# Performance work log

Measured on AMD Instinct MI355X. Metric: run time of the kernel, lower is better.

The kernel has to match this reference:

```python
import jax, jax.numpy as jnp
import numpy as np

B, S, D = 2, 2048, 2048
H, KVH, HD = 32, 8, 64
GROUPS = H // KVH  # 4
NEG = -1e9


def setup_inputs() -> dict:
    key = jax.random.key(0)
    ks = jax.random.split(key, 5)
    x = jax.random.normal(ks[0], (B, S, D), dtype=jnp.float32)
    # causal additive mask [1,1,S,S]
    causal = jnp.triu(jnp.full((S, S), NEG, dtype=jnp.float32), k=1)[None, None]
    Wq = jax.random.normal(ks[1], (D, D), dtype=jnp.float32) * (D ** -0.5)
    Wk = jax.random.normal(ks[2], (KVH * HD, D), dtype=jnp.float32) * (D ** -0.5)
    Wv = jax.random.normal(ks[3], (KVH * HD, D), dtype=jnp.float32) * (D ** -0.5)
    Wo = jax.random.normal(ks[4], (D, D), dtype=jnp.float32) * (D ** -0.5)
    return {"x": x, "attention_mask": causal, "Wq": Wq, "Wk": Wk, "Wv": Wv, "Wo": Wo}


def reference(x, attention_mask, Wq, Wk, Wv, Wo):
    b, s, _ = x.shape
    # projections (nn.Linear: y = x @ W.T)
    q = (x @ Wq.T).reshape(b, s, H, HD).transpose(0, 2, 1, 3)      # [b,H,s,hd]
    k = (x @ Wk.T).reshape(b, s, KVH, HD).transpose(0, 2, 1, 3)    # [b,KVH,s,hd]
    v = (x @ Wv.T).reshape(b, s, KVH, HD).transpose(0, 2, 1, 3)
    new_kv_cache = (k, v)
    # repeat_interleave over head dim for GQA
    k = jnp.repeat(k, GROUPS, axis=1)  # [b,H,s,hd]
    v = jnp.repeat(v, GROUPS, axis=1)
    scale = 1.0 / jnp.sqrt(jnp.float32(HD))
    scores = jnp.einsum('bhqd,bhkd->bhqk', q, k) * scale
    scores = scores + attention_mask
    attn = jax.nn.softmax(scores.astype(jnp.float32), axis=-1).astype(q.dtype)
    out = jnp.einsum('bhqk,bhkd->bhqd', attn, v)  # [b,H,s,hd]
    out = out.transpose(0, 2, 1, 3).reshape(b, s, H * HD)
    output = out @ Wo.T
    return (output, new_kv_cache[0], new_kv_cache[1])
```

## Files before the change

kernel.cpp:

```cpp
#include <hip/hip_runtime.h>
#include <hip/hip_bf16.h>
#include <stdint.h>

#define B_ 2
#define S_ 2048
#define D_ 2048
#define H_ 32
#define KVH_ 8
#define HD_ 64

typedef __bf16 bf16x8 __attribute__((ext_vector_type(8)));
typedef float f32x4 __attribute__((ext_vector_type(4)));

#define MFMA16(a, b, c) __builtin_amdgcn_mfma_f32_16x16x32_bf16((a), (b), (c), 0, 0, 0)

typedef __attribute__((address_space(1))) void gvoid_t;
typedef __attribute__((address_space(3))) void lvoid_t;

__device__ __forceinline__ void async_ld16(__hip_bfloat16* lds, const __hip_bfloat16* g) {
  __builtin_amdgcn_global_load_lds((gvoid_t*)(void*)(g), (lvoid_t*)(lds), 16, 0, 0);
}

__device__ __forceinline__ unsigned short f2bu(float f) {
  __hip_bfloat16 h = __float2bfloat16(f);
  return *reinterpret_cast<unsigned short*>(&h);
}

__global__ void cast_all_kernel(const float* __restrict__ x,
                                const float* __restrict__ wq,
                                const float* __restrict__ wk,
                                const float* __restrict__ wv,
                                const float* __restrict__ wo,
                                unsigned short* __restrict__ xb,
                                unsigned short* __restrict__ wqkvb,
                                unsigned short* __restrict__ wob) {
  constexpr int NX = B_ * S_ * D_ / 4;
  constexpr int NQ = D_ * D_ / 4;
  constexpr int NK = KVH_ * HD_ * D_ / 4;
  constexpr int E0 = NX;
  constexpr int E1 = E0 + NQ;
  constexpr int E2 = E1 + NK;
  constexpr int E3 = E2 + NK;
  constexpr int E4 = E3 + NQ;
  const int stride = gridDim.x * blockDim.x;
  for (int i = blockIdx.x * blockDim.x + threadIdx.x; i < E4; i += stride) {
    const float* src; unsigned short* dst; int j;
    if (i < E0)      { src = x;  dst = xb;                              j = i; }
    else if (i < E1) { src = wq; dst = wqkvb;                           j = i - E0; }
    else if (i < E2) { src = wk; dst = wqkvb + (size_t)2048 * D_;       j = i - E1; }
    else if (i < E3) { src = wv; dst = wqkvb + (size_t)2560 * D_;       j = i - E2; }
    else             { src = wo; dst = wob;                             j = i - E3; }
    float4 v = reinterpret_cast<const float4*>(src)[j];
    ushort4 o;
    o.x = f2bu(v.x); o.y = f2bu(v.y); o.z = f2bu(v.z); o.w = f2bu(v.w);
    reinterpret_cast<ushort4*>(dst)[j] = o;
  }
}

template <int MODE>
__global__ __launch_bounds__(256, 2)
void gemm_bt(const __hip_bfloat16* __restrict__ A,
             const __hip_bfloat16* __restrict__ W,
             float* __restrict__ Cf, __hip_bfloat16* __restrict__ Cb,
             float* __restrict__ Cf2, __hip_bfloat16* __restrict__ Cb2,
             __hip_bfloat16* __restrict__ Cb3,
             int M, int N, int K) {
  __shared__ __align__(16) __hip_bfloat16 sA[128 * 32];
  __shared__ __align__(16) __hip_bfloat16 sB[128 * 32];
  const int tid = threadIdx.x;
  const int lane = tid & 63;
  const int wv = tid >> 6;
  const int l15 = lane & 15, l4 = lane >> 4;
  const int bm = blockIdx.x * 128, bn = blockIdx.y * 128;
  const int wm = (wv >> 1) * 64, wn = (wv & 1) * 64;

  const int ci0 = tid, ci1 = tid + 256;
  const __hip_bfloat16* gA0 = A + (size_t)(bm + (ci0 >> 2)) * K + (ci0 & 3) * 8;
  const __hip_bfloat16* gA1 = A + (size_t)(bm + (ci1 >> 2)) * K + (ci1 & 3) * 8;
  const __hip_bfloat16* gB0 = W + (size_t)(bn + (ci0 >> 2)) * K + (ci0 & 3) * 8;
  const __hip_bfloat16* gB1 = W + (size_t)(bn + (ci1 >> 2)) * K + (ci1 & 3) * 8;
  __hip_bfloat16* lA0 = &sA[ci0 * 8];
  __hip_bfloat16* lA1 = &sA[ci1 * 8];
  __hip_bfloat16* lB0 = &sB[ci0 * 8];
  __hip_bfloat16* lB1 = &sB[ci1 * 8];

  f32x4 acc[4][4];
#pragma unroll
  for (int i = 0; i < 4; ++i) {
#pragma unroll
    for (int j = 0; j < 4; ++j) acc[i][j] = f32x4{0.f, 0.f, 0.f, 0.f};
  }

  for (int k0 = 0; k0 < K; k0 += 32) {
    async_ld16(lA0, gA0 + k0);
    async_ld16(lA1, gA1 + k0);
    async_ld16(lB0, gB0 + k0);
    async_ld16(lB1, gB1 + k0);
    __syncthreads();
    bf16x8 af[4], bfr[4];
#pragma unroll
    for (int i = 0; i < 4; ++i)
      af[i] = *reinterpret_cast<const bf16x8*>(&sA[(wm + i * 16 + l15) * 32 + l4 * 8]);
#pragma unroll
    for (int j = 0; j < 4; ++j)
      bfr[j] = *reinterpret_cast<const bf16x8*>(&sB[(wn + j * 16 + l15) * 32 + l4 * 8]);
#pragma unroll
    for (int i = 0; i < 4; ++i) {
#pragma unroll
      for (int j = 0; j < 4; ++j) acc[i][j] = MFMA16(af[i], bfr[j], acc[i][j]);
    }
    __syncthreads();
  }

#pragma unroll
  for (int i = 0; i < 4; ++i) {
#pragma unroll
    for (int j = 0; j < 4; ++j) {
      const int col = bn + wn + j * 16 + l15;
#pragma unroll
      for (int r = 0; r < 4; ++r) {
        const int row = bm + wm + i * 16 + l4 * 4 + r;
        const float v = acc[i][j][r];
        if (MODE == 1) {
          Cf[(size_t)row * N + col] = v;
        } else {
          if (bn < 2048) {
            Cb[(size_t)row * 2048 + col] = __float2bfloat16(v);
          } else {
            const int bb = row >> 11, s = row & 2047;
            const int kv = col - 2048;
            if (kv < 512) {
              const int g = kv >> 6, hd = kv & 63;
              const size_t idx = ((size_t)(bb * KVH_ + g) * S_ + s) * HD_ + hd;
              Cf[idx] = v;
              Cb2[idx] = __float2bfloat16(v);
            } else {
              const int vv = kv - 512;
              const int g = vv >> 6, hd = vv & 63;
              const size_t idx = ((size_t)(bb * KVH_ + g) * S_ + s) * HD_ + hd;
              Cf2[idx] = v;
              Cb3[((size_t)(bb * KVH_ + g) * HD_ + hd) * S_ + s] = __float2bfloat16(v);
            }
          }
        }
      }
    }
  }
}

__global__ __launch_bounds__(512, 4)
void attn_fused(const __hip_bfloat16* __restrict__ Qb,
                const __hip_bfloat16* __restrict__ Kb,
                const __hip_bfloat16* __restrict__ Vtb,
                __hip_bfloat16* __restrict__ AOb) {
  __shared__ __align__(16) __hip_bfloat16 sK[2][64 * 64];
  __shared__ __align__(16) __hip_bfloat16 sV[2][64 * 64];
  __shared__ __align__(16) __hip_bfloat16 sP[8 * 32 * 64];

  const int tid = threadIdx.x;
  const int lane = tid & 63;
  const int wv = tid >> 6;
  const int l15 = lane & 15, l4 = lane >> 4;
  const int qa = blockIdx.x;
  const int qb = 15 - qa;
  const int isB = wv >> 2;
  const int wq = wv & 3;
  const int qt = isB ? qb : qa;
  const int h = blockIdx.y;
  const int b = blockIdx.z;
  const int g = h >> 2;

  bf16x8 qf[2][2];
  {
    const __hip_bfloat16* Qp =
        Qb + ((size_t)(b * S_ + qt * 128 + wq * 32)) * D_ + h * HD_;
#pragma unroll
    for (int i = 0; i < 2; ++i) {
#pragma unroll
      for (int c = 0; c < 2; ++c) {
        qf[i][c] = *reinterpret_cast<const bf16x8*>(
            Qp + (size_t)(i * 16 + l15) * D_ + c * 32 + l4 * 8);
      }
    }
  }

  f32x4 oacc[2][4];
  f32x4 lacc[2];
#pragma unroll
  for (int i = 0; i < 2; ++i) {
    lacc[i] = f32x4{0.f, 0.f, 0.f, 0.f};
#pragma unroll
    for (int j = 0; j < 4; ++j) oacc[i][j] = f32x4{0.f, 0.f, 0.f, 0.f};
  }

  bf16x8 vone;
#pragma unroll
  for (int j = 0; j < 8; ++j) vone[j] = (__bf16)1.0f;

  const __hip_bfloat16* Kp = Kb + (size_t)(b * KVH_ + g) * S_ * HD_;
  const __hip_bfloat16* Vp = Vtb + (size_t)(b * KVH_ + g) * HD_ * S_;
  __hip_bfloat16* sPw = sP + wv * (32 * 64);
  const float CE = 0.125f * 1.4426950408889634f;
  const float MSUB = 8.0f;

  const int r0 = tid >> 3, c0 = (tid & 7) ^ (r0 & 7);
  const __hip_bfloat16* gk = Kp + (size_t)r0 * HD_ + c0 * 8;
  const __hip_bfloat16* gv = Vp + (size_t)r0 * S_ + c0 * 8;

  auto stage = [&](int buf) {
    async_ld16(&sK[buf][tid * 8], gk);
    async_ld16(&sV[buf][tid * 8], gv);
    gk += 64 * HD_;
    gv += 64;
  };

  auto pack = [&](f32x4 (&sc)[2][4], int koff) {
    if (koff >= 0) {
#pragma unroll
      for (int i = 0; i < 2; ++i) {
#pragma unroll
        for (int jn = 0; jn < 4; ++jn) {
          const int kp = koff + jn * 16 + l15;
#pragma unroll
          for (int r = 0; r < 4; ++r) {
            const int qp = wq * 32 + i * 16 + l4 * 4 + r;
            if (kp > qp) sc[i][jn][r] = -3.0e38f;
          }
        }
      }
    }
#pragma unroll
    for (int i = 0; i < 2; ++i) {
#pragma unroll
      for (int jj = 0; jj < 4; ++jj) {
#pragma unroll
        for (int r = 0; r < 4; ++r) {
          const float p = exp2f(fmaf(sc[i][jj][r], CE, -MSUB));
          sPw[(i * 16 + l4 * 4 + r) * 64 + ((jj ^ l4) * 16 + l15)] =
              __float2bfloat16(p);
        }
      }
    }
  };

  const int nsteps = 2 * qb + 2;
  const int kmax = isB ? nsteps : (2 * qa + 2);
  stage(0);
  for (int ki = 0; ki < nsteps; ++ki) {
    const int cur = ki & 1;
    __syncthreads();
    if (ki + 1 < nsteps) stage(cur ^ 1);
    if (ki < kmax) {
      const int ko = ((ki >> 1) == qt) ? (ki & 1) * 64 : -1;

      f32x4 sc[2][4];
      __builtin_amdgcn_s_setprio(1);
#pragma unroll
      for (int jn = 0; jn < 4; ++jn) {
        const int row = jn * 16 + l15;
        const bf16x8 k0 = *reinterpret_cast<const bf16x8*>(
            &sK[cur][(row * 8 + (l4 ^ (row & 7))) * 8]);
        const bf16x8 k1 = *reinterpret_cast<const bf16x8*>(
            &sK[cur][(row * 8 + ((4 + l4) ^ (row & 7))) * 8]);
#pragma unroll
        for (int i = 0; i < 2; ++i) {
          f32x4 t = f32x4{0.f, 0.f, 0.f, 0.f};
          t = MFMA16(qf[i][0], k0, t);
          t = MFMA16(qf[i][1], k1, t);
          sc[i][jn] = t;
        }
      }
      __builtin_amdgcn_s_setprio(0);

      pack(sc, ko);

      const int gr = (l15 >> 2) & 3;
      __builtin_amdgcn_s_setprio(1);
#pragma unroll
      for (int kc = 0; kc < 2; ++kc) {
        bf16x8 vf[4];
#pragma unroll
        for (int jn = 0; jn < 4; ++jn) {
          const int row = jn * 16 + l15;
          vf[jn] = *reinterpret_cast<const bf16x8*>(
              &sV[cur][(row * 8 + ((kc * 4 + l4) ^ (row & 7))) * 8]);
        }
        const int pcol = (((kc * 2 + (l4 >> 1)) ^ gr) * 16 + (l4 & 1) * 8);
#pragma unroll
        for (int i = 0; i < 2; ++i) {
          const bf16x8 pf = *reinterpret_cast<const bf16x8*>(
              &sPw[(i * 16 + l15) * 64 + pcol]);
#pragma unroll
          for (int jn = 0; jn < 4; ++jn) oacc[i][jn] = MFMA16(pf, vf[jn], oacc[i][jn]);
          lacc[i] = MFMA16(pf, vone, lacc[i]);
        }
      }
      __builtin_amdgcn_s_setprio(0);
    }
  }

#pragma unroll
  for (int i = 0; i < 2; ++i) {
    float inv[4];
#pragma unroll
    for (int r = 0; r < 4; ++r) inv[r] = 1.0f / lacc[i][r];
#pragma unroll
    for (int jn = 0; jn < 4; ++jn) {
#pragma unroll
      for (int r = 0; r < 4; ++r) {
        const int qp = qt * 128 + wq * 32 + i * 16 + l4 * 4 + r;
        AOb[(size_t)(b * S_ + qp) * D_ + h * HD_ + jn * 16 + l15] =
            __float2bfloat16(oacc[i][jn][r] * inv[r]);
      }
    }
  }
}

extern "C" void kernel_launch(void* const* d_in, const int* in_sizes, int n_in,
                              void* d_out, int out_size, void* d_ws, size_t ws_size,
                              hipStream_t stream) {
  (void)in_sizes; (void)n_in; (void)out_size; (void)ws_size;
  const float* x = (const float*)d_in[0];
  const float* Wq = (const float*)d_in[2];
  const float* Wk = (const float*)d_in[3];
  const float* Wv = (const float*)d_in[4];
  const float* Wo = (const float*)d_in[5];

  float* outO = (float*)d_out;
  float* outK = outO + (size_t)B_ * S_ * D_;
  float* outV = outK + (size_t)B_ * KVH_ * S_ * HD_;

  char* p = (char*)d_ws;
  __hip_bfloat16* xb    = (__hip_bfloat16*)p; p += (size_t)B_ * S_ * D_ * 2;
  __hip_bfloat16* Wqkvb = (__hip_bfloat16*)p; p += (size_t)3072 * D_ * 2;
  __hip_bfloat16* Wob   = (__hip_bfloat16*)p; p += (size_t)D_ * D_ * 2;
  __hip_bfloat16* Qbf   = (__hip_bfloat16*)p; p += (size_t)B_ * S_ * D_ * 2;
  __hip_bfloat16* Kbf   = (__hip_bfloat16*)p; p += (size_t)B_ * KVH_ * S_ * HD_ * 2;
  __hip_bfloat16* Vtb   = (__hip_bfloat16*)p; p += (size_t)B_ * KVH_ * S_ * HD_ * 2;
  __hip_bfloat16* AOb   = (__hip_bfloat16*)p; p += (size_t)B_ * S_ * D_ * 2;

  cast_all_kernel<<<dim3(4096), dim3(256), 0, stream>>>(
      x, Wq, Wk, Wv, Wo,
      (unsigned short*)xb, (unsigned short*)Wqkvb, (unsigned short*)Wob);

  gemm_bt<4><<<dim3(32, 24), dim3(256), 0, stream>>>(
      xb, Wqkvb, outK, Qbf, outV, Kbf, Vtb, 4096, 3072, 2048);
  attn_fused<<<dim3(8, 32, 2), dim3(512), 0, stream>>>(Qbf, Kbf, Vtb, AOb);
  gemm_bt<1><<<dim3(32, 16), dim3(256), 0, stream>>>(
      AOb, Wob, outO, nullptr, nullptr, nullptr, nullptr, 4096, 2048, 2048);
}
```

Baseline: 322.5 us.

## Replace paired causal q-tiles with one 128-row q-tile per block, heaviest first

Each attention block used to pair two complementary 128-row query tiles (qa and 15-qa) across 8 waves, with each wave owning 32 rows. Now each block handles a single 128-row tile with 8 waves of 16 rows each, and the grid is reordered so the longest causal tiles launch first (qt = 15 - blockIdx.y). This doubles the block count, halves per-wave registers and the P staging buffer, and relies on longest-first scheduling instead of pairing for load balance. The trade is that K/V tiles are reloaded per block for half as many query rows and each MFMA K-fragment load is reused by one row group instead of two.

```diff
diff --git a/kernel.cpp b/kernel.cpp
--- a/kernel.cpp
+++ b/kernel.cpp
@@ -155,43 +155,30 @@
                 __hip_bfloat16* __restrict__ AOb) {
   __shared__ __align__(16) __hip_bfloat16 sK[2][64 * 64];
   __shared__ __align__(16) __hip_bfloat16 sV[2][64 * 64];
-  __shared__ __align__(16) __hip_bfloat16 sP[8 * 32 * 64];
+  __shared__ __align__(16) __hip_bfloat16 sP[8 * 16 * 64];
 
   const int tid = threadIdx.x;
   const int lane = tid & 63;
   const int wv = tid >> 6;
   const int l15 = lane & 15, l4 = lane >> 4;
-  const int qa = blockIdx.x;
-  const int qb = 15 - qa;
-  const int isB = wv >> 2;
-  const int wq = wv & 3;
-  const int qt = isB ? qb : qa;
-  const int h = blockIdx.y;
-  const int b = blockIdx.z;
+  const int h = blockIdx.x & 31;
+  const int b = blockIdx.x >> 5;
+  const int qt = 15 - blockIdx.y;
   const int g = h >> 2;
 
-  bf16x8 qf[2][2];
+  bf16x8 qf[2];
   {
     const __hip_bfloat16* Qp =
-        Qb + ((size_t)(b * S_ + qt * 128 + wq * 32)) * D_ + h * HD_;
-#pragma unroll
-    for (int i = 0; i < 2; ++i) {
-#pragma unroll
-      for (int c = 0; c < 2; ++c) {
-        qf[i][c] = *reinterpret_cast<const bf16x8*>(
-            Qp + (size_t)(i * 16 + l15) * D_ + c * 32 + l4 * 8);
-      }
-    }
-  }
-
-  f32x4 oacc[2][4];
-  f32x4 lacc[2];
-#pragma unroll
-  for (int i = 0; i < 2; ++i) {
-    lacc[i] = f32x4{0.f, 0.f, 0.f, 0.f};
-#pragma unroll
-    for (int j = 0; j < 4; ++j) oacc[i][j] = f32x4{0.f, 0.f, 0.f, 0.f};
-  }
+        Qb + ((size_t)(b * S_ + qt * 128 + wv * 16 + l15)) * D_ + h * HD_;
+#pragma unroll
+    for (int c = 0; c < 2; ++c)
+      qf[c] = *reinterpret_cast<const bf16x8*>(Qp + c * 32 + l4 * 8);
+  }
+
+  f32x4 oacc[4];
+  f32x4 lacc = f32x4{0.f, 0.f, 0.f, 0.f};
+#pragma unroll
+  for (int j = 0; j < 4; ++j) oacc[j] = f32x4{0.f, 0.f, 0.f, 0.f};
 
   bf16x8 vone;
 #pragma unroll
@@ -199,7 +186,7 @@
 
   const __hip_bfloat16* Kp = Kb + (size_t)(b * KVH_ + g) * S_ * HD_;
   const __hip_bfloat16* Vp = Vtb + (size_t)(b * KVH_ + g) * HD_ * S_;
-  __hip_bfloat16* sPw = sP + wv * (32 * 64);
+  __hip_bfloat16* sPw = sP + wv * (16 * 64);
   const float CE = 0.125f * 1.4426950408889634f;
   const float MSUB = 8.0f;
 
@@ -214,104 +201,84 @@
     gv += 64;
   };
 
-  auto pack = [&](f32x4 (&sc)[2][4], int koff) {
+  auto pack = [&](f32x4 (&sc)[4], int koff) {
     if (koff >= 0) {
 #pragma unroll
-      for (int i = 0; i < 2; ++i) {
-#pragma unroll
-        for (int jn = 0; jn < 4; ++jn) {
-          const int kp = koff + jn * 16 + l15;
-#pragma unroll
-          for (int r = 0; r < 4; ++r) {
-            const int qp = wq * 32 + i * 16 + l4 * 4 + r;
-            if (kp > qp) sc[i][jn][r] = -3.0e38f;
-          }
+      for (int jn = 0; jn < 4; ++jn) {
+        const int kp = koff + jn * 16 + l15;
+#pragma unroll
+        for (int r = 0; r < 4; ++r) {
+          const int qp = wv * 16 + l4 * 4 + r;
+          if (kp > qp) sc[jn][r] = -3.0e38f;
         }
       }
     }
 #pragma unroll
-    for (int i = 0; i < 2; ++i) {
-#pragma unroll
-      for (int jj = 0; jj < 4; ++jj) {
-#pragma unroll
-        for (int r = 0; r < 4; ++r) {
-          const float p = exp2f(fmaf(sc[i][jj][r], CE, -MSUB));
-          sPw[(i * 16 + l4 * 4 + r) * 64 + ((jj ^ l4) * 16 + l15)] =
-              __float2bfloat16(p);
-        }
+    for (int jj = 0; jj < 4; ++jj) {
+#pragma unroll
+      for (int r = 0; r < 4; ++r) {
+        const float p = exp2f(fmaf(sc[jj][r], CE, -MSUB));
+        sPw[(l4 * 4 + r) * 64 + ((jj ^ l4) * 16 + l15)] = __float2bfloat16(p);
       }
     }
   };
 
-  const int nsteps = 2 * qb + 2;
-  const int kmax = isB ? nsteps : (2 * qa + 2);
+  const int nsteps = 2 * qt + 2;
   stage(0);
   for (int ki = 0; ki < nsteps; ++ki) {
     const int cur = ki & 1;
     __syncthreads();
     if (ki + 1 < nsteps) stage(cur ^ 1);
-    if (ki < kmax) {
-      const int ko = ((ki >> 1) == qt) ? (ki & 1) * 64 : -1;
-
-      f32x4 sc[2][4];
-      __builtin_amdgcn_s_setprio(1);
+    const int ko = ((ki >> 1) == qt) ? (ki & 1) * 64 : -1;
+
+    f32x4 sc[4];
+    __builtin_amdgcn_s_setprio(1);
+#pragma unroll
+    for (int jn = 0; jn < 4; ++jn) {
+      const int row = jn * 16 + l15;
+      const bf16x8 k0 = *reinterpret_cast<const bf16x8*>(
+          &sK[cur][(row * 8 + (l4 ^ (row & 7))) * 8]);
+      const bf16x8 k1 = *reinterpret_cast<const bf16x8*>(
+          &sK[cur][(row * 8 + ((4 + l4) ^ (row & 7))) * 8]);
+      f32x4 t = f32x4{0.f, 0.f, 0.f, 0.f};
+      t = MFMA16(qf[0], k0, t);
+      t = MFMA16(qf[1], k1, t);
+      sc[jn] = t;
+    }
+    __builtin_amdgcn_s_setprio(0);
+
+    pack(sc, ko);
+
+    const int gr = (l15 >> 2) & 3;
+    __builtin_amdgcn_s_setprio(1);
+#pragma unroll
+    for (int kc = 0; kc < 2; ++kc) {
+      bf16x8 vf[4];
 #pragma unroll
       for (int jn = 0; jn < 4; ++jn) {
         const int row = jn * 16 + l15;
-        const bf16x8 k0 = *reinterpret_cast<const bf16x8*>(
-            &sK[cur][(row * 8 + (l4 ^ (row & 7))) * 8]);
-        const bf16x8 k1 = *reinterpret_cast<const bf16x8*>(
-            &sK[cur][(row * 8 + ((4 + l4) ^ (row & 7))) * 8]);
-#pragma unroll
-        for (int i = 0; i < 2; ++i) {
-          f32x4 t = f32x4{0.f, 0.f, 0.f, 0.f};
-          t = MFMA16(qf[i][0], k0, t);
-          t = MFMA16(qf[i][1], k1, t);
-          sc[i][jn] = t;
-        }
+        vf[jn] = *reinterpret_cast<const bf16x8*>(
+            &sV[cur][(row * 8 + ((kc * 4 + l4) ^ (row & 7))) * 8]);
       }
-      __builtin_amdgcn_s_setprio(0);
-
-      pack(sc, ko);
-
-      const int gr = (l15 >> 2) & 3;
-      __builtin_amdgcn_s_setprio(1);
-#pragma unroll
-      for (int kc = 0; kc < 2; ++kc) {
-        bf16x8 vf[4];
-#pragma unroll
-        for (int jn = 0; jn < 4; ++jn) {
-          const int row = jn * 16 + l15;
-          vf[jn] = *reinterpret_cast<const bf16x8*>(
-              &sV[cur][(row * 8 + ((kc * 4 + l4) ^ (row & 7))) * 8]);
-        }
-        const int pcol = (((kc * 2 + (l4 >> 1)) ^ gr) * 16 + (l4 & 1) * 8);
-#pragma unroll
-        for (int i = 0; i < 2; ++i) {
-          const bf16x8 pf = *reinterpret_cast<const bf16x8*>(
-              &sPw[(i * 16 + l15) * 64 + pcol]);
-#pragma unroll
-          for (int jn = 0; jn < 4; ++jn) oacc[i][jn] = MFMA16(pf, vf[jn], oacc[i][jn]);
-          lacc[i] = MFMA16(pf, vone, lacc[i]);
-        }
-      }
-      __builtin_amdgcn_s_setprio(0);
-    }
-  }
-
-#pragma unroll
-  for (int i = 0; i < 2; ++i) {
-    float inv[4];
-#pragma unroll
-    for (int r = 0; r < 4; ++r) inv[r] = 1.0f / lacc[i][r];
-#pragma unroll
-    for (int jn = 0; jn < 4; ++jn) {
-#pragma unroll
-      for (int r = 0; r < 4; ++r) {
-        const int qp = qt * 128 + wq * 32 + i * 16 + l4 * 4 + r;
-        AOb[(size_t)(b * S_ + qp) * D_ + h * HD_ + jn * 16 + l15] =
-            __float2bfloat16(oacc[i][jn][r] * inv[r]);
-      }
+      const int pcol = (((kc * 2 + (l4 >> 1)) ^ gr) * 16 + (l4 & 1) * 8);
+      const bf16x8 pf = *reinterpret_cast<const bf16x8*>(&sPw[l15 * 64 + pcol]);
+#pragma unroll
+      for (int jn = 0; jn < 4; ++jn) oacc[jn] = MFMA16(pf, vf[jn], oacc[jn]);
+      lacc = MFMA16(pf, vone, lacc);
+    }
+    __builtin_amdgcn_s_setprio(0);
+  }
+
+  float inv[4];
+#pragma unroll
+  for (int r = 0; r < 4; ++r) inv[r] = 1.0f / lacc[r];
+#pragma unroll
+  for (int jn = 0; jn < 4; ++jn) {
+#pragma unroll
+    for (int r = 0; r < 4; ++r) {
+      const int qp = qt * 128 + wv * 16 + l4 * 4 + r;
+      AOb[(size_t)(b * S_ + qp) * D_ + h * HD_ + jn * 16 + l15] =
+          __float2bfloat16(oacc[jn][r] * inv[r]);
     }
   }
 }
@@ -345,7 +312,7 @@
 
   gemm_bt<4><<<dim3(32, 24), dim3(256), 0, stream>>>(
       xb, Wqkvb, outK, Qbf, outV, Kbf, Vtb, 4096, 3072, 2048);
-  attn_fused<<<dim3(8, 32, 2), dim3(512), 0, stream>>>(Qbf, Kbf, Vtb, AOb);
+  attn_fused<<<dim3(64, 16, 1), dim3(512), 0, stream>>>(Qbf, Kbf, Vtb, AOb);
   gemm_bt<1><<<dim3(32, 16), dim3(256), 0, stream>>>(
       AOb, Wob, outO, nullptr, nullptr, nullptr, nullptr, 4096, 2048, 2048);
 }
```

Measured after the change: 308.7 us. 1.04x faster.
